# Kernel optimization log

Hardware: AMD Instinct MI355X
Metric: run time of the kernel (lower is better)

The kernel has to match this reference:

```python
import jax, jax.numpy as jnp
import numpy as np

N_NODES = 100000
N_EDGES = 200000
IN_FEATS = 1024
H_FEATS = 512
N_HEADS = 4
HEAD_DIM = H_FEATS // N_HEADS  # 128
N_CLASSES = 2983
BATCH = 1024


def setup_inputs() -> dict:
    key = jax.random.key(0)
    ks = jax.random.split(key, 24)
    x = jax.random.normal(ks[0], (N_NODES, IN_FEATS), jnp.float32)
    e1_src = jax.random.randint(ks[1], (N_EDGES,), 0, N_NODES)
    e1_dst = jax.random.randint(ks[2], (N_EDGES,), 0, N_NODES)
    e2_src = jax.random.randint(ks[3], (N_EDGES,), 0, N_NODES)
    e2_dst = jax.random.randint(ks[4], (N_EDGES,), 0, N_NODES)

    def lin_w(k, fin, fout):
        return jax.random.normal(k, (fin, fout), jnp.float32) * np.float32(1.0 / np.sqrt(fin))

    def att_w(k):
        return jax.random.normal(k, (N_HEADS, HEAD_DIM), jnp.float32) * np.float32(0.1)

    inp = dict(x=x, e1_src=e1_src, e1_dst=e1_dst, e2_src=e2_src, e2_dst=e2_dst,
               batch_size=BATCH)
    # layer 0 (in_feats -> h_feats), one GATConv per edge type
    inp["w0a"] = lin_w(ks[5], IN_FEATS, H_FEATS); inp["as0a"] = att_w(ks[6]); inp["ad0a"] = att_w(ks[7]); inp["b0a"] = jnp.zeros((H_FEATS,), jnp.float32)
    inp["w0b"] = lin_w(ks[8], IN_FEATS, H_FEATS); inp["as0b"] = att_w(ks[9]); inp["ad0b"] = att_w(ks[10]); inp["b0b"] = jnp.zeros((H_FEATS,), jnp.float32)
    # layer 1 (h_feats -> h_feats)
    inp["w1a"] = lin_w(ks[11], H_FEATS, H_FEATS); inp["as1a"] = att_w(ks[12]); inp["ad1a"] = att_w(ks[13]); inp["b1a"] = jnp.zeros((H_FEATS,), jnp.float32)
    inp["w1b"] = lin_w(ks[14], H_FEATS, H_FEATS); inp["as1b"] = att_w(ks[15]); inp["ad1b"] = att_w(ks[16]); inp["b1b"] = jnp.zeros((H_FEATS,), jnp.float32)
    # classification head
    inp["lin_w"] = lin_w(ks[17], H_FEATS, N_CLASSES)
    inp["lin_b"] = jnp.zeros((N_CLASSES,), jnp.float32)
    return inp


def gat_conv(x, src, dst, W, a_src, a_dst, b):
    """PyG GATConv (add_self_loops=False, concat=True, attn negative_slope=0.2)."""
    h = (x @ W).reshape(-1, N_HEADS, HEAD_DIM)          # [N, H, C]
    alpha_src = jnp.einsum('nhc,hc->nh', h, a_src)       # [N, H]
    alpha_dst = jnp.einsum('nhc,hc->nh', h, a_dst)       # [N, H]
    e = jax.nn.leaky_relu(alpha_src[src] + alpha_dst[dst], 0.2)   # [E, H]
    # segment softmax over incoming edges of each destination node
    m = jax.ops.segment_max(e, dst, num_segments=N_NODES)          # [N, H]
    ex = jnp.exp(e - m[dst])
    denom = jax.ops.segment_sum(ex, dst, num_segments=N_NODES)     # [N, H]
    alpha = ex / denom[dst]                                        # [E, H]
    msg = alpha[:, :, None] * h[src]                               # [E, H, C]
    out = jax.ops.segment_sum(msg, dst, num_segments=N_NODES)      # [N, H, C]
    return out.reshape(-1, N_HEADS * HEAD_DIM) + b


def reference(x, e1_src, e1_dst, e2_src, e2_dst, batch_size,
              w0a, as0a, ad0a, b0a, w0b, as0b, ad0b, b0b,
              w1a, as1a, ad1a, b1a, w1b, as1b, ad1b, b1b,
              lin_w, lin_b):
    # layer 0: HeteroConv sums per-edge-type GATConv outputs on 'paper'
    h1 = gat_conv(x, e1_src, e1_dst, w0a, as0a, ad0a, b0a) \
       + gat_conv(x, e2_src, e2_dst, w0b, as0b, ad0b, b0b)
    h1 = jax.nn.leaky_relu(h1, 0.01)   # F.leaky_relu default slope; dropout is identity in eval
    # layer 1
    h2 = gat_conv(h1, e1_src, e1_dst, w1a, as1a, ad1a, b1a) \
       + gat_conv(h1, e2_src, e2_dst, w1b, as1b, ad1b, b1b)
    # classification head on the seed nodes
    return h2[:batch_size] @ lin_w + lin_b
```

## Files before the change

### kernel.cpp

```cpp
#include <hip/hip_runtime.h>

#define N_NODES 100000
#define N_EDGES 200000
#define IN_FEATS 1024
#define H_FEATS 512
#define N_HEADS 4
#define HEAD_DIM 128
#define N_CLASSES 2983
#define BATCH 1024
#define NCHUNK2 782

typedef __attribute__((ext_vector_type(8))) short short8;
typedef __attribute__((ext_vector_type(4))) float floatx4;

typedef __attribute__((address_space(1))) void global_as_void;
typedef __attribute__((address_space(3))) void lds_as_void;

__device__ __forceinline__ float bf2f(unsigned short u) {
    union { unsigned int i; float f; } x; x.i = ((unsigned int)u) << 16; return x.f;
}
__device__ __forceinline__ unsigned short f2bf(float f) {
    union { float f; unsigned int i; } x; x.f = f;
    unsigned int r = x.i + 0x7FFFu + ((x.i >> 16) & 1u);
    return (unsigned short)(r >> 16);
}
__device__ __forceinline__ void load_lds16(const void* g, void* l) {
    __builtin_amdgcn_global_load_lds((const global_as_void*)g, (lds_as_void*)l, 16, 0, 0);
}

__global__ __launch_bounds__(256, 3)
void gemm_kernel(const void* __restrict__ Ain, int a_fp32, int a_dense,
                 const unsigned short* __restrict__ BT,
                 void* __restrict__ Cout, const float* __restrict__ bias,
                 const float* __restrict__ att_s, const float* __restrict__ att_d,
                 const float* __restrict__ att_s2, const float* __restrict__ att_d2,
                 float* __restrict__ asrc, float* __restrict__ adst,
                 const int* __restrict__ rowlist, const int* __restrict__ countp,
                 int M, int N, int n_tiles, int K, int out_bf16)
{
    __shared__ __attribute__((aligned(16))) unsigned short As[128 * 32];
    __shared__ __attribute__((aligned(16))) unsigned short Bs[128 * 32];
    __shared__ float attbuf[128][4];
    const int tid  = threadIdx.x;
    const int lane = tid & 63;
    const int wave = tid >> 6;
    const int bid = blockIdx.x;
    int mt, nt;
    if (n_tiles == 8) {
        mt = (bid & 7) + ((bid >> 6) << 3);
        nt = (bid >> 3) & 7;
    } else {
        mt = bid / n_tiles;
        nt = bid - mt * n_tiles;
    }
    const int m0 = mt * 128;
    const int n0 = nt * 128;
    int Mv = M;
    if (countp) Mv = countp[0];
    if (m0 >= Mv) return;
    const int wr = (wave >> 1) * 64;
    const int wc = (wave & 1) * 64;
    const int lm = lane & 15;
    const int quad = lane >> 4;

    auto arow = [&](int r) -> int {
        int gr = m0 + r; if (gr > Mv - 1) gr = Mv - 1;
        if (rowlist && !a_dense) gr = rowlist[gr];
        return gr;
    };

    const float* a_fp[2];
    const unsigned short* a_bf[2];
    char* a_lds[2];
    const unsigned short* b_bf[2];
    char* b_lds[2];
    if (a_fp32) {
        int row = tid >> 2, slot = tid & 3;
#pragma unroll
        for (int p = 0; p < 2; p++) {
            int r = p * 64 + row;
            a_fp[p] = (const float*)Ain + (size_t)arow(r) * K + (slot ^ ((r >> 1) & 3)) * 8;
        }
    } else {
#pragma unroll
        for (int i = 0; i < 2; i++) {
            int r = wave * 32 + i * 16 + (lane >> 2);
            a_bf[i] = (const unsigned short*)Ain + (size_t)arow(r) * K
                    + ((lane & 3) ^ ((r >> 1) & 3)) * 8;
            a_lds[i] = (char*)As + (size_t)(wave * 2 + i) * 1024;
        }
    }
#pragma unroll
    for (int i = 0; i < 2; i++) {
        int r = wave * 32 + i * 16 + (lane >> 2);
        int gn = n0 + r; if (gn > N - 1) gn = N - 1;
        b_bf[i] = BT + (size_t)gn * K + ((lane & 3) ^ ((r >> 1) & 3)) * 8;
        b_lds[i] = (char*)Bs + (size_t)(wave * 2 + i) * 1024;
    }

    floatx4 acc[4][4];
#pragma unroll
    for (int i = 0; i < 4; i++)
#pragma unroll
        for (int j = 0; j < 4; j++) acc[i][j] = (floatx4)0.0f;

    for (int k0 = 0; k0 < K; k0 += 32) {
        __syncthreads();
        if (a_fp32) {
            int row = tid >> 2, slot = tid & 3;
#pragma unroll
            for (int p = 0; p < 2; p++) {
                int r = p * 64 + row;
                floatx4 f0 = *(const floatx4*)(a_fp[p] + k0);
                floatx4 f1 = *(const floatx4*)(a_fp[p] + k0 + 4);
                short8 v;
                v[0] = (short)f2bf(f0[0]); v[1] = (short)f2bf(f0[1]);
                v[2] = (short)f2bf(f0[2]); v[3] = (short)f2bf(f0[3]);
                v[4] = (short)f2bf(f1[0]); v[5] = (short)f2bf(f1[1]);
                v[6] = (short)f2bf(f1[2]); v[7] = (short)f2bf(f1[3]);
                *(short8*)&As[r * 32 + slot * 8] = v;
            }
        } else {
#pragma unroll
            for (int i = 0; i < 2; i++)
                load_lds16(a_bf[i] + k0, a_lds[i]);
        }
#pragma unroll
        for (int i = 0; i < 2; i++)
            load_lds16(b_bf[i] + k0, b_lds[i]);
        __syncthreads();
        short8 af[4], bfr[4];
#pragma unroll
        for (int i = 0; i < 4; i++) {
            int ra = wr + i * 16 + lm;
            af[i] = *(const short8*)&As[ra * 32 + ((quad ^ ((ra >> 1) & 3)) << 3)];
            int rb = wc + i * 16 + lm;
            bfr[i] = *(const short8*)&Bs[rb * 32 + ((quad ^ ((rb >> 1) & 3)) << 3)];
        }
#pragma unroll
        for (int i = 0; i < 4; i++)
#pragma unroll
            for (int j = 0; j < 4; j++)
                acc[i][j] = __builtin_amdgcn_mfma_f32_16x16x32_bf16(af[i], bfr[j], acc[i][j], 0, 0, 0);
    }

    if (att_s) {
        const int h = nt;
        const float* wsp = (h < 4) ? att_s : att_s2;
        const float* wdp = (h < 4) ? att_d : att_d2;
        const int hh = h & 3;
        const int half2 = (wc >> 6) * 2;
#pragma unroll
        for (int i = 0; i < 4; i++) {
#pragma unroll
            for (int r = 0; r < 4; r++) {
                float ss = 0.f, sd = 0.f;
#pragma unroll
                for (int j = 0; j < 4; j++) {
                    int c = wc + j * 16 + lm;
                    ss += acc[i][j][r] * wsp[hh * HEAD_DIM + c];
                    sd += acc[i][j][r] * wdp[hh * HEAD_DIM + c];
                }
#pragma unroll
                for (int off = 1; off < 16; off <<= 1) {
                    ss += __shfl_xor(ss, off);
                    sd += __shfl_xor(sd, off);
                }
                if (lm == 0) {
                    int rl = wr + i * 16 + quad * 4 + r;
                    attbuf[rl][half2]     = ss;
                    attbuf[rl][half2 + 1] = sd;
                }
            }
        }
        __syncthreads();
        if (tid < 128) {
            int grl = m0 + tid;
            if (grl < Mv) {
                int gr = rowlist ? rowlist[grl] : grl;
                asrc[(size_t)gr * 8 + h] = attbuf[tid][0] + attbuf[tid][2];
                adst[(size_t)gr * 8 + h] = attbuf[tid][1] + attbuf[tid][3];
            }
        }
    }

#pragma unroll
    for (int i = 0; i < 4; i++) {
        int grb = wr + i * 16 + quad * 4;
#pragma unroll
        for (int j = 0; j < 4; j++) {
            int gc = n0 + wc + j * 16 + lm;
            if (gc < N) {
#pragma unroll
                for (int r = 0; r < 4; r++) {
                    int grl = m0 + grb + r;
                    if (grl < Mv) {
                        int gr = rowlist ? rowlist[grl] : grl;
                        float v = acc[i][j][r];
                        if (out_bf16) {
                            ((unsigned short*)Cout)[(size_t)gr * N + gc] = f2bf(v);
                        } else {
                            float b = bias ? bias[gc] : 0.0f;
                            ((float*)Cout)[(size_t)gr * N + gc] = v + b;
                        }
                    }
                }
            }
        }
    }
}

__global__ void prep1_kernel(const float* __restrict__ w0a, const float* __restrict__ w0b,
                             const float* __restrict__ w1a, const float* __restrict__ w1b,
                             const float* __restrict__ linw,
                             unsigned short* __restrict__ WT0, unsigned short* __restrict__ WT1,
                             unsigned short* __restrict__ WTl,
                             const int* __restrict__ e1s, const int* __restrict__ e1d,
                             const int* __restrict__ e2s, const int* __restrict__ e2d,
                             int* __restrict__ flag1, int* __restrict__ cnt2)
{
    const int gsz = gridDim.x * 256;
    const int gid = blockIdx.x * 256 + threadIdx.x;
    for (int i = gid; i < 1024 * 1024; i += gsz) {
        int n = i >> 10, k = i & 1023;
        const float* W = (n < 512) ? w0a : w0b;
        WT0[i] = f2bf(W[(size_t)k * 512 + (n & 511)]);
    }
    for (int i = gid; i < 1024 * 512; i += gsz) {
        int n = i >> 9, k = i & 511;
        const float* W = (n < 512) ? w1a : w1b;
        WT1[i] = f2bf(W[(size_t)k * 512 + (n & 511)]);
    }
    for (int i = gid; i < N_CLASSES * 512; i += gsz) {
        int n = i >> 9, k = i & 511;
        WTl[i] = f2bf(linw[(size_t)k * N_CLASSES + n]);
    }
    for (int e = gid; e < N_EDGES; e += gsz) {
        if (e < BATCH) flag1[e] = 1;
        int d1 = e1d[e], d2 = e2d[e];
        if (d1 < BATCH) flag1[e1s[e]] = 1;
        if (d2 < BATCH) flag1[e2s[e]] = 1;
        atomicAdd(&cnt2[d1], 1);
        atomicAdd(&cnt2[N_NODES + d2], 1);
    }
}

__global__ void mark0_kernel(const int* __restrict__ e1s, const int* __restrict__ e1d,
                             const int* __restrict__ e2s, const int* __restrict__ e2d,
                             const int* __restrict__ flag1, int* __restrict__ flag0,
                             int E, int Nn)
{
    int i = blockIdx.x * blockDim.x + threadIdx.x;
    if (i < E) {
        if (flag1[e1d[i]]) flag0[e1s[i]] = 1;
        if (flag1[e2d[i]]) flag0[e2s[i]] = 1;
    }
    if (i < Nn && flag1[i]) flag0[i] = 1;
}

__global__ void scanA_kernel(const int* __restrict__ flagbuf, const int* __restrict__ cnt2,
                             int* __restrict__ partialF, int* __restrict__ chunkF,
                             int* __restrict__ partialC, int* __restrict__ chunkC)
{
    __shared__ int sm[256];
    int b = blockIdx.x;
    const int* src; int* pdst; int* cdst; int cb;
    if (b < NCHUNK2) { src = flagbuf; pdst = partialF; cdst = chunkF; cb = b; }
    else             { src = cnt2;    pdst = partialC; cdst = chunkC; cb = b - NCHUNK2; }
    int t = threadIdx.x;
    int i = cb * 256 + t;
    int v = (i < 2 * N_NODES) ? src[i] : 0;
    sm[t] = v; __syncthreads();
    int val = v;
#pragma unroll
    for (int off = 1; off < 256; off <<= 1) {
        int u = (t >= off) ? sm[t - off] : 0;
        __syncthreads();
        val += u; sm[t] = val;
        __syncthreads();
    }
    if (i < 2 * N_NODES) pdst[i] = val - v;
    if (t == 255) cdst[cb] = val;
}

__global__ void scanB_kernel(int* __restrict__ chunkF, int* __restrict__ chunkC, int n)
{
    __shared__ int sm[1024];
    int t = threadIdx.x;
#pragma unroll
    for (int pass = 0; pass < 2; pass++) {
        int* c = pass ? chunkC : chunkF;
        int v = (t < n) ? c[t] : 0;
        sm[t] = v; __syncthreads();
        int val = v;
#pragma unroll
        for (int off = 1; off < 1024; off <<= 1) {
            int u = (t >= off) ? sm[t - off] : 0;
            __syncthreads();
            val += u; sm[t] = val;
            __syncthreads();
        }
        if (t < n) c[t] = val - v;
        __syncthreads();
    }
}

__global__ void finalize_kernel(const int* __restrict__ flagbuf,
                                const int* __restrict__ partialF, const int* __restrict__ chunkF,
                                const int* __restrict__ partialC, const int* __restrict__ chunkC,
                                int* __restrict__ list1, int* __restrict__ list0,
                                int* __restrict__ count1, int* __restrict__ count0,
                                int* __restrict__ rowptrc, int* __restrict__ cursor)
{
    int i = blockIdx.x * 256 + threadIdx.x;
    if (i >= 2 * N_NODES) return;
    int r = partialC[i] + chunkC[i >> 8];
    rowptrc[i] = r;
    cursor[i] = r;
    if (i == 0) rowptrc[2 * N_NODES] = 2 * N_EDGES;
    int total1 = partialF[N_NODES] + chunkF[N_NODES >> 8];
    int pos = partialF[i] + chunkF[i >> 8];
    int f = flagbuf[i];
    if (i < N_NODES) {
        if (f) list1[pos] = i;
        if (i == 0) count1[0] = total1;
    } else {
        if (f) list0[pos - total1] = i - N_NODES;
        if (i == 2 * N_NODES - 1) count0[0] = pos + f - total1;
    }
}

__global__ void fill_cvt_kernel(const int* __restrict__ e1s, const int* __restrict__ e1d,
                                const int* __restrict__ e2s, const int* __restrict__ e2d,
                                int* __restrict__ cursor, int* __restrict__ srcsc,
                                const float* __restrict__ X, const int* __restrict__ list0,
                                const int* __restrict__ count0, unsigned short* __restrict__ Y)
{
    const int gsz = gridDim.x * 256;
    const int gid = blockIdx.x * 256 + threadIdx.x;
    for (int e = gid; e < N_EDGES; e += gsz) {
        int p = atomicAdd(&cursor[e1d[e]], 1);
        srcsc[p] = e1s[e];
        int q = atomicAdd(&cursor[N_NODES + e2d[e]], 1);
        srcsc[q] = e2s[e];
    }
    int n0 = count0[0];
    int col = (threadIdx.x & 127) * 8;
    for (int i = blockIdx.x * 2 + (threadIdx.x >> 7); i < n0; i += gridDim.x * 2) {
        const floatx4* xp = (const floatx4*)(X + (size_t)list0[i] * IN_FEATS + col);
        floatx4 f0 = xp[0], f1 = xp[1];
        short8 v;
        v[0] = (short)f2bf(f0[0]); v[1] = (short)f2bf(f0[1]);
        v[2] = (short)f2bf(f0[2]); v[3] = (short)f2bf(f0[3]);
        v[4] = (short)f2bf(f1[0]); v[5] = (short)f2bf(f1[1]);
        v[6] = (short)f2bf(f1[2]); v[7] = (short)f2bf(f1[3]);
        *(short8*)(Y + (size_t)i * IN_FEATS + col) = v;
    }
}

__global__ void gather2_kernel(const int* __restrict__ rowptrc, const int* __restrict__ srcsc,
                               const float* __restrict__ asrc, const float* __restrict__ adst,
                               const unsigned short* __restrict__ H,
                               const float* __restrict__ b1, const float* __restrict__ b2,
                               const int* __restrict__ dlist, const int* __restrict__ dcountp,
                               unsigned short* __restrict__ Out, int ndst, int do_lrelu)
{
    int nd = dcountp ? dcountp[0] : ndst;
    int lane = threadIdx.x & 63;
    int head = lane >> 4;
    int col = lane * 8;
    for (int i = blockIdx.x * 4 + (threadIdx.x >> 6); i < nd; i += gridDim.x * 4) {
        int d = dlist ? dlist[i] : i;
        float r[8], acc[8];
        {
            int beg = rowptrc[d], end = rowptrc[d + 1];
            float ad = adst[(size_t)d * 8 + head];
            float den = 0.f;
#pragma unroll
            for (int k = 0; k < 8; k++) acc[k] = 0.f;
            for (int j = beg; j < end; j++) {
                int s = srcsc[j];
                float v = asrc[(size_t)s * 8 + head] + ad;
                v = v > 0.f ? v : 0.2f * v;
                float ex = expf(v);
                den += ex;
                short8 hv = *(const short8*)(H + (size_t)s * 1024 + col);
#pragma unroll
                for (int k = 0; k < 8; k++) acc[k] += ex * bf2f((unsigned short)hv[k]);
            }
            float inv = den > 0.f ? 1.f / den : 0.f;
#pragma unroll
            for (int k = 0; k < 8; k++) r[k] = acc[k] * inv;
        }
        {
            int beg = rowptrc[N_NODES + d], end = rowptrc[N_NODES + d + 1];
            float ad = adst[(size_t)d * 8 + 4 + head];
            float den = 0.f;
#pragma unroll
            for (int k = 0; k < 8; k++) acc[k] = 0.f;
            for (int j = beg; j < end; j++) {
                int s = srcsc[j];
                float v = asrc[(size_t)s * 8 + 4 + head] + ad;
                v = v > 0.f ? v : 0.2f * v;
                float ex = expf(v);
                den += ex;
                short8 hv = *(const short8*)(H + (size_t)s * 1024 + 512 + col);
#pragma unroll
                for (int k = 0; k < 8; k++) acc[k] += ex * bf2f((unsigned short)hv[k]);
            }
            float inv = den > 0.f ? 1.f / den : 0.f;
#pragma unroll
            for (int k = 0; k < 8; k++) r[k] += acc[k] * inv;
        }
        short8 o;
#pragma unroll
        for (int k = 0; k < 8; k++) {
            float f = r[k] + b1[col + k] + b2[col + k];
            if (do_lrelu) f = f > 0.f ? f : 0.01f * f;
            o[k] = (short)f2bf(f);
        }
        *(short8*)(Out + (size_t)i * 512 + col) = o;
    }
}

extern "C" void kernel_launch(void* const* d_in, const int* in_sizes, int n_in,
                              void* d_out, int out_size, void* d_ws, size_t ws_size,
                              hipStream_t stream)
{
    const float* x    = (const float*)d_in[0];
    const int* e1s    = (const int*)d_in[1];
    const int* e1d    = (const int*)d_in[2];
    const int* e2s    = (const int*)d_in[3];
    const int* e2d    = (const int*)d_in[4];
    const float* w0a  = (const float*)d_in[6];
    const float* as0a = (const float*)d_in[7];
    const float* ad0a = (const float*)d_in[8];
    const float* b0a  = (const float*)d_in[9];
    const float* w0b  = (const float*)d_in[10];
    const float* as0b = (const float*)d_in[11];
    const float* ad0b = (const float*)d_in[12];
    const float* b0b  = (const float*)d_in[13];
    const float* w1a  = (const float*)d_in[14];
    const float* as1a = (const float*)d_in[15];
    const float* ad1a = (const float*)d_in[16];
    const float* b1a  = (const float*)d_in[17];
    const float* w1b  = (const float*)d_in[18];
    const float* as1b = (const float*)d_in[19];
    const float* ad1b = (const float*)d_in[20];
    const float* b1b  = (const float*)d_in[21];
    const float* linw = (const float*)d_in[22];
    const float* linb = (const float*)d_in[23];
    float* out = (float*)d_out;
    (void)in_sizes; (void)n_in; (void)out_size;

    char* ws = (char*)d_ws;
    size_t off = 0;
    auto carve = [&](size_t bytes) -> void* {
        void* p = ws + off; off += (bytes + 255) & ~(size_t)255; return p;
    };
    unsigned short* WT0 = (unsigned short*)carve((size_t)2 * H_FEATS * IN_FEATS * 2);
    unsigned short* WT1 = (unsigned short*)carve((size_t)2 * H_FEATS * H_FEATS * 2);
    unsigned short* WTl = (unsigned short*)carve((size_t)N_CLASSES * H_FEATS * 2);
    unsigned short* Hbf = (unsigned short*)carve((size_t)N_NODES * 1024 * 2);
    unsigned short* H1c = (unsigned short*)carve((size_t)N_NODES * H_FEATS * 2);
    unsigned short* h2s = (unsigned short*)carve((size_t)BATCH * H_FEATS * 2);
    float* asrc = (float*)carve((size_t)N_NODES * 8 * 4);
    float* adst = (float*)carve((size_t)N_NODES * 8 * 4);
    int* cnt2    = (int*)carve((size_t)2 * N_NODES * 4);
    int* flagbuf = (int*)carve((size_t)2 * N_NODES * 4);
    int* rowptrc = (int*)carve((size_t)(2 * N_NODES + 1) * 4);
    int* srcsc   = (int*)carve((size_t)2 * N_EDGES * 4);
    int* partialF= (int*)carve((size_t)2 * N_NODES * 4);
    int* partialC= (int*)carve((size_t)2 * N_NODES * 4);
    int* chunkF  = (int*)carve((size_t)1024 * 4);
    int* chunkC  = (int*)carve((size_t)1024 * 4);
    int* list1   = (int*)carve((size_t)N_NODES * 4);
    int* list0   = (int*)carve((size_t)N_NODES * 4);
    int* count1  = (int*)carve(256);
    int* count0  = (int*)carve(256);
    unsigned short* xc = nullptr;
    {
        size_t need = (size_t)N_NODES * IN_FEATS * 2;
        if (off + need <= ws_size) xc = (unsigned short*)carve(need);
    }

    const int MT8 = (((N_NODES + 127) / 128) + 7) & ~7;
    const int EG = (N_EDGES + 255) / 256;

    hipMemsetAsync(cnt2, 0, (size_t)4 * N_NODES * 4, stream);
    prep1_kernel<<<2048, 256, 0, stream>>>(w0a, w0b, w1a, w1b, linw, WT0, WT1, WTl,
                                           e1s, e1d, e2s, e2d, flagbuf, cnt2);
    mark0_kernel<<<EG, 256, 0, stream>>>(e1s, e1d, e2s, e2d, flagbuf, flagbuf + N_NODES,
                                         N_EDGES, N_NODES);
    scanA_kernel<<<2 * NCHUNK2, 256, 0, stream>>>(flagbuf, cnt2, partialF, chunkF, partialC, chunkC);
    scanB_kernel<<<1, 1024, 0, stream>>>(chunkF, chunkC, NCHUNK2);
    finalize_kernel<<<NCHUNK2, 256, 0, stream>>>(flagbuf, partialF, chunkF, partialC, chunkC,
                                                 list1, list0, count1, count0, rowptrc, cnt2);
    fill_cvt_kernel<<<1024, 256, 0, stream>>>(e1s, e1d, e2s, e2d, cnt2, srcsc,
                                              x, list0, count0, xc ? xc : (unsigned short*)Hbf);

    if (xc) {
        gemm_kernel<<<MT8 * 8, 256, 0, stream>>>(xc, 0, 1, WT0, Hbf, nullptr,
                                                 as0a, ad0a, as0b, ad0b, asrc, adst,
                                                 list0, count0,
                                                 N_NODES, 1024, 8, IN_FEATS, 1);
    } else {
        gemm_kernel<<<MT8 * 8, 256, 0, stream>>>(x, 1, 0, WT0, Hbf, nullptr,
                                                 as0a, ad0a, as0b, ad0b, asrc, adst,
                                                 list0, count0,
                                                 N_NODES, 1024, 8, IN_FEATS, 1);
    }
    gather2_kernel<<<2048, 256, 0, stream>>>(rowptrc, srcsc, asrc, adst, Hbf, b0a, b0b,
                                             list1, count1, H1c, N_NODES, 1);
    gemm_kernel<<<MT8 * 8, 256, 0, stream>>>(H1c, 0, 1, WT1, Hbf, nullptr,
                                             as1a, ad1a, as1b, ad1b, asrc, adst,
                                             list1, count1,
                                             N_NODES, 1024, 8, H_FEATS, 1);
    gather2_kernel<<<256, 256, 0, stream>>>(rowptrc, srcsc, asrc, adst, Hbf, b1a, b1b,
                                            nullptr, nullptr, h2s, BATCH, 0);
    const int HN_T = (N_CLASSES + 127) / 128;
    gemm_kernel<<<(BATCH / 128) * HN_T, 256, 0, stream>>>(h2s, 0, 0, WTl, out, linb,
                                                          nullptr, nullptr, nullptr, nullptr,
                                                          nullptr, nullptr, nullptr, nullptr,
                                                          BATCH, N_CLASSES, HN_T, H_FEATS, 0);
}
```

Before: 749.0 us.

## Fuse preprocessing kernels into one cooperative kernel and double GEMM K-step

Six preprocessing launches plus a memset (weight transpose, flag marking, scans, CSR finalize, edge fill, x conversion) are merged into one cooperative kernel that separates phases with grid-wide syncs. This removes launch gaps and per-kernel tail effects. The GEMM main loop now loads two 32-wide K slices per iteration into doubled LDS buffers, halving the barrier count per tile. The trade-offs are more LDS per block, which may lower GEMM occupancy, and a 512-block cooperative grid that runs less parallel work in each phase than the old launches did.

```diff
diff --git a/kernel.cpp b/kernel.cpp
--- a/kernel.cpp
+++ b/kernel.cpp
@@ -1,4 +1,5 @@
 #include <hip/hip_runtime.h>
+#include <hip/hip_cooperative_groups.h>
 
 #define N_NODES 100000
 #define N_EDGES 200000
@@ -38,8 +39,8 @@
                  const int* __restrict__ rowlist, const int* __restrict__ countp,
                  int M, int N, int n_tiles, int K, int out_bf16)
 {
-    __shared__ __attribute__((aligned(16))) unsigned short As[128 * 32];
-    __shared__ __attribute__((aligned(16))) unsigned short Bs[128 * 32];
+    __shared__ __attribute__((aligned(16))) unsigned short As[2][128 * 32];
+    __shared__ __attribute__((aligned(16))) unsigned short Bs[2][128 * 32];
     __shared__ float attbuf[128][4];
     const int tid  = threadIdx.x;
     const int lane = tid & 63;
@@ -87,7 +88,7 @@
             int r = wave * 32 + i * 16 + (lane >> 2);
             a_bf[i] = (const unsigned short*)Ain + (size_t)arow(r) * K
                     + ((lane & 3) ^ ((r >> 1) & 3)) * 8;
-            a_lds[i] = (char*)As + (size_t)(wave * 2 + i) * 1024;
+            a_lds[i] = (char*)&As[0][0] + (size_t)(wave * 2 + i) * 1024;
         }
     }
 #pragma unroll
@@ -95,7 +96,7 @@
         int r = wave * 32 + i * 16 + (lane >> 2);
         int gn = n0 + r; if (gn > N - 1) gn = N - 1;
         b_bf[i] = BT + (size_t)gn * K + ((lane & 3) ^ ((r >> 1) & 3)) * 8;
-        b_lds[i] = (char*)Bs + (size_t)(wave * 2 + i) * 1024;
+        b_lds[i] = (char*)&Bs[0][0] + (size_t)(wave * 2 + i) * 1024;
     }
 
     floatx4 acc[4][4];
@@ -104,44 +105,54 @@
 #pragma unroll
         for (int j = 0; j < 4; j++) acc[i][j] = (floatx4)0.0f;
 
-    for (int k0 = 0; k0 < K; k0 += 32) {
+    for (int k0 = 0; k0 < K; k0 += 64) {
         __syncthreads();
         if (a_fp32) {
             int row = tid >> 2, slot = tid & 3;
 #pragma unroll
+            for (int pp = 0; pp < 2; pp++)
+#pragma unroll
             for (int p = 0; p < 2; p++) {
                 int r = p * 64 + row;
-                floatx4 f0 = *(const floatx4*)(a_fp[p] + k0);
-                floatx4 f1 = *(const floatx4*)(a_fp[p] + k0 + 4);
+                const float* ap = a_fp[p] + k0 + pp * 32;
+                floatx4 f0 = *(const floatx4*)ap;
+                floatx4 f1 = *(const floatx4*)(ap + 4);
                 short8 v;
                 v[0] = (short)f2bf(f0[0]); v[1] = (short)f2bf(f0[1]);
                 v[2] = (short)f2bf(f0[2]); v[3] = (short)f2bf(f0[3]);
                 v[4] = (short)f2bf(f1[0]); v[5] = (short)f2bf(f1[1]);
                 v[6] = (short)f2bf(f1[2]); v[7] = (short)f2bf(f1[3]);
-                *(short8*)&As[r * 32 + slot * 8] = v;
+                *(short8*)&As[pp][r * 32 + slot * 8] = v;
             }
         } else {
 #pragma unroll
+            for (int pp = 0; pp < 2; pp++)
+#pragma unroll
             for (int i = 0; i < 2; i++)
-                load_lds16(a_bf[i] + k0, a_lds[i]);
-        }
+                load_lds16(a_bf[i] + k0 + pp * 32, a_lds[i] + pp * 8192);
+        }
+#pragma unroll
+        for (int pp = 0; pp < 2; pp++)
 #pragma unroll
         for (int i = 0; i < 2; i++)
-            load_lds16(b_bf[i] + k0, b_lds[i]);
+            load_lds16(b_bf[i] + k0 + pp * 32, b_lds[i] + pp * 8192);
         __syncthreads();
-        short8 af[4], bfr[4];
-#pragma unroll
-        for (int i = 0; i < 4; i++) {
-            int ra = wr + i * 16 + lm;
-            af[i] = *(const short8*)&As[ra * 32 + ((quad ^ ((ra >> 1) & 3)) << 3)];
-            int rb = wc + i * 16 + lm;
-            bfr[i] = *(const short8*)&Bs[rb * 32 + ((quad ^ ((rb >> 1) & 3)) << 3)];
-        }
-#pragma unroll
-        for (int i = 0; i < 4; i++)
-#pragma unroll
-            for (int j = 0; j < 4; j++)
-                acc[i][j] = __builtin_amdgcn_mfma_f32_16x16x32_bf16(af[i], bfr[j], acc[i][j], 0, 0, 0);
+#pragma unroll
+        for (int pp = 0; pp < 2; pp++) {
+            short8 af[4], bfr[4];
+#pragma unroll
+            for (int i = 0; i < 4; i++) {
+                int ra = wr + i * 16 + lm;
+                af[i] = *(const short8*)&As[pp][ra * 32 + ((quad ^ ((ra >> 1) & 3)) << 3)];
+                int rb = wc + i * 16 + lm;
+                bfr[i] = *(const short8*)&Bs[pp][rb * 32 + ((quad ^ ((rb >> 1) & 3)) << 3)];
+            }
+#pragma unroll
+            for (int i = 0; i < 4; i++)
+#pragma unroll
+                for (int j = 0; j < 4; j++)
+                    acc[i][j] = __builtin_amdgcn_mfma_f32_16x16x32_bf16(af[i], bfr[j], acc[i][j], 0, 0, 0);
+        }
     }
 
     if (att_s) {
@@ -210,151 +221,145 @@
     }
 }
 
-__global__ void prep1_kernel(const float* __restrict__ w0a, const float* __restrict__ w0b,
-                             const float* __restrict__ w1a, const float* __restrict__ w1b,
-                             const float* __restrict__ linw,
-                             unsigned short* __restrict__ WT0, unsigned short* __restrict__ WT1,
-                             unsigned short* __restrict__ WTl,
-                             const int* __restrict__ e1s, const int* __restrict__ e1d,
-                             const int* __restrict__ e2s, const int* __restrict__ e2d,
-                             int* __restrict__ flag1, int* __restrict__ cnt2)
+struct PrepArgs {
+    const float *w0a, *w0b, *w1a, *w1b, *linw;
+    unsigned short *WT0, *WT1, *WTl;
+    const int *e1s, *e1d, *e2s, *e2d;
+    int *flagbuf, *cnt2;
+    int *partialF, *chunkF, *partialC, *chunkC;
+    int *list1, *list0, *count1, *count0;
+    int *rowptrc, *srcsc;
+    const float* x;
+    unsigned short* xc;
+};
+
+__global__ __launch_bounds__(256, 2)
+void prep_all_kernel(PrepArgs a)
 {
+    cooperative_groups::grid_group g = cooperative_groups::this_grid();
     const int gsz = gridDim.x * 256;
     const int gid = blockIdx.x * 256 + threadIdx.x;
+    const int t = threadIdx.x;
+    __shared__ int sm[1024];
+    __shared__ int ts[256];
+
+    for (int i = gid; i < 4 * N_NODES; i += gsz) a.cnt2[i] = 0;
+    g.sync();
+
     for (int i = gid; i < 1024 * 1024; i += gsz) {
         int n = i >> 10, k = i & 1023;
-        const float* W = (n < 512) ? w0a : w0b;
-        WT0[i] = f2bf(W[(size_t)k * 512 + (n & 511)]);
+        const float* W = (n < 512) ? a.w0a : a.w0b;
+        a.WT0[i] = f2bf(W[(size_t)k * 512 + (n & 511)]);
     }
     for (int i = gid; i < 1024 * 512; i += gsz) {
         int n = i >> 9, k = i & 511;
-        const float* W = (n < 512) ? w1a : w1b;
-        WT1[i] = f2bf(W[(size_t)k * 512 + (n & 511)]);
+        const float* W = (n < 512) ? a.w1a : a.w1b;
+        a.WT1[i] = f2bf(W[(size_t)k * 512 + (n & 511)]);
     }
     for (int i = gid; i < N_CLASSES * 512; i += gsz) {
         int n = i >> 9, k = i & 511;
-        WTl[i] = f2bf(linw[(size_t)k * N_CLASSES + n]);
+        a.WTl[i] = f2bf(a.linw[(size_t)k * N_CLASSES + n]);
     }
     for (int e = gid; e < N_EDGES; e += gsz) {
-        if (e < BATCH) flag1[e] = 1;
-        int d1 = e1d[e], d2 = e2d[e];
-        if (d1 < BATCH) flag1[e1s[e]] = 1;
-        if (d2 < BATCH) flag1[e2s[e]] = 1;
-        atomicAdd(&cnt2[d1], 1);
-        atomicAdd(&cnt2[N_NODES + d2], 1);
-    }
-}
-
-__global__ void mark0_kernel(const int* __restrict__ e1s, const int* __restrict__ e1d,
-                             const int* __restrict__ e2s, const int* __restrict__ e2d,
-                             const int* __restrict__ flag1, int* __restrict__ flag0,
-                             int E, int Nn)
-{
-    int i = blockIdx.x * blockDim.x + threadIdx.x;
-    if (i < E) {
-        if (flag1[e1d[i]]) flag0[e1s[i]] = 1;
-        if (flag1[e2d[i]]) flag0[e2s[i]] = 1;
-    }
-    if (i < Nn && flag1[i]) flag0[i] = 1;
-}
-
-__global__ void scanA_kernel(const int* __restrict__ flagbuf, const int* __restrict__ cnt2,
-                             int* __restrict__ partialF, int* __restrict__ chunkF,
-                             int* __restrict__ partialC, int* __restrict__ chunkC)
-{
-    __shared__ int sm[256];
-    int b = blockIdx.x;
-    const int* src; int* pdst; int* cdst; int cb;
-    if (b < NCHUNK2) { src = flagbuf; pdst = partialF; cdst = chunkF; cb = b; }
-    else             { src = cnt2;    pdst = partialC; cdst = chunkC; cb = b - NCHUNK2; }
-    int t = threadIdx.x;
-    int i = cb * 256 + t;
-    int v = (i < 2 * N_NODES) ? src[i] : 0;
-    sm[t] = v; __syncthreads();
-    int val = v;
-#pragma unroll
-    for (int off = 1; off < 256; off <<= 1) {
-        int u = (t >= off) ? sm[t - off] : 0;
-        __syncthreads();
-        val += u; sm[t] = val;
-        __syncthreads();
-    }
-    if (i < 2 * N_NODES) pdst[i] = val - v;
-    if (t == 255) cdst[cb] = val;
-}
-
-__global__ void scanB_kernel(int* __restrict__ chunkF, int* __restrict__ chunkC, int n)
-{
-    __shared__ int sm[1024];
-    int t = threadIdx.x;
-#pragma unroll
-    for (int pass = 0; pass < 2; pass++) {
-        int* c = pass ? chunkC : chunkF;
-        int v = (t < n) ? c[t] : 0;
+        if (e < BATCH) a.flagbuf[e] = 1;
+        int d1 = a.e1d[e], d2 = a.e2d[e];
+        if (d1 < BATCH) a.flagbuf[a.e1s[e]] = 1;
+        if (d2 < BATCH) a.flagbuf[a.e2s[e]] = 1;
+        atomicAdd(&a.cnt2[d1], 1);
+        atomicAdd(&a.cnt2[N_NODES + d2], 1);
+    }
+    g.sync();
+
+    for (int e = gid; e < N_EDGES; e += gsz) {
+        if (a.flagbuf[a.e1d[e]]) a.flagbuf[N_NODES + a.e1s[e]] = 1;
+        if (a.flagbuf[a.e2d[e]]) a.flagbuf[N_NODES + a.e2s[e]] = 1;
+    }
+    for (int i = gid; i < N_NODES; i += gsz)
+        if (a.flagbuf[i]) a.flagbuf[N_NODES + i] = 1;
+    g.sync();
+
+    for (int c = blockIdx.x; c < 2 * NCHUNK2; c += gridDim.x) {
+        const int* src; int* pdst; int* cdst; int cb;
+        if (c < NCHUNK2) { src = a.flagbuf; pdst = a.partialF; cdst = a.chunkF; cb = c; }
+        else             { src = a.cnt2;    pdst = a.partialC; cdst = a.chunkC; cb = c - NCHUNK2; }
+        int i = cb * 256 + t;
+        int v = (i < 2 * N_NODES) ? src[i] : 0;
         sm[t] = v; __syncthreads();
         int val = v;
 #pragma unroll
-        for (int off = 1; off < 1024; off <<= 1) {
+        for (int off = 1; off < 256; off <<= 1) {
             int u = (t >= off) ? sm[t - off] : 0;
             __syncthreads();
             val += u; sm[t] = val;
             __syncthreads();
         }
-        if (t < n) c[t] = val - v;
+        if (i < 2 * N_NODES) pdst[i] = val - v;
+        if (t == 255) cdst[cb] = val;
         __syncthreads();
     }
-}
-
-__global__ void finalize_kernel(const int* __restrict__ flagbuf,
-                                const int* __restrict__ partialF, const int* __restrict__ chunkF,
-                                const int* __restrict__ partialC, const int* __restrict__ chunkC,
-                                int* __restrict__ list1, int* __restrict__ list0,
-                                int* __restrict__ count1, int* __restrict__ count0,
-                                int* __restrict__ rowptrc, int* __restrict__ cursor)
-{
-    int i = blockIdx.x * 256 + threadIdx.x;
-    if (i >= 2 * N_NODES) return;
-    int r = partialC[i] + chunkC[i >> 8];
-    rowptrc[i] = r;
-    cursor[i] = r;
-    if (i == 0) rowptrc[2 * N_NODES] = 2 * N_EDGES;
-    int total1 = partialF[N_NODES] + chunkF[N_NODES >> 8];
-    int pos = partialF[i] + chunkF[i >> 8];
-    int f = flagbuf[i];
-    if (i < N_NODES) {
-        if (f) list1[pos] = i;
-        if (i == 0) count1[0] = total1;
-    } else {
-        if (f) list0[pos - total1] = i - N_NODES;
-        if (i == 2 * N_NODES - 1) count0[0] = pos + f - total1;
-    }
-}
-
-__global__ void fill_cvt_kernel(const int* __restrict__ e1s, const int* __restrict__ e1d,
-                                const int* __restrict__ e2s, const int* __restrict__ e2d,
-                                int* __restrict__ cursor, int* __restrict__ srcsc,
-                                const float* __restrict__ X, const int* __restrict__ list0,
-                                const int* __restrict__ count0, unsigned short* __restrict__ Y)
-{
-    const int gsz = gridDim.x * 256;
-    const int gid = blockIdx.x * 256 + threadIdx.x;
+    g.sync();
+
+    if (blockIdx.x == 0) {
+        for (int pass = 0; pass < 2; pass++) {
+            int* c = pass ? a.chunkC : a.chunkF;
+            for (int i = t; i < 1024; i += 256) sm[i] = (i < NCHUNK2) ? c[i] : 0;
+            __syncthreads();
+            int b4 = t * 4;
+            int a0 = sm[b4], a1 = sm[b4 + 1], a2 = sm[b4 + 2], a3 = sm[b4 + 3];
+            int s1 = a0, s2 = s1 + a1, s3 = s2 + a2, tot = s3 + a3;
+            ts[t] = tot; __syncthreads();
+            int val = tot;
+#pragma unroll
+            for (int off = 1; off < 256; off <<= 1) {
+                int u = (t >= off) ? ts[t - off] : 0;
+                __syncthreads();
+                val += u; ts[t] = val;
+                __syncthreads();
+            }
+            int exc = val - tot;
+            sm[b4] = exc; sm[b4 + 1] = exc + s1; sm[b4 + 2] = exc + s2; sm[b4 + 3] = exc + s3;
+            __syncthreads();
+            for (int i = t; i < NCHUNK2; i += 256) c[i] = sm[i];
+            __syncthreads();
+        }
+    }
+    g.sync();
+
+    for (int i = gid; i < 2 * N_NODES; i += gsz) {
+        int r = a.partialC[i] + a.chunkC[i >> 8];
+        a.rowptrc[i] = r;
+        a.cnt2[i] = r;
+        if (i == 0) a.rowptrc[2 * N_NODES] = 2 * N_EDGES;
+        int total1 = a.partialF[N_NODES] + a.chunkF[N_NODES >> 8];
+        int pos = a.partialF[i] + a.chunkF[i >> 8];
+        int f = a.flagbuf[i];
+        if (i < N_NODES) {
+            if (f) a.list1[pos] = i;
+            if (i == 0) a.count1[0] = total1;
+        } else {
+            if (f) a.list0[pos - total1] = i - N_NODES;
+            if (i == 2 * N_NODES - 1) a.count0[0] = pos + f - total1;
+        }
+    }
+    g.sync();
+
     for (int e = gid; e < N_EDGES; e += gsz) {
-        int p = atomicAdd(&cursor[e1d[e]], 1);
-        srcsc[p] = e1s[e];
-        int q = atomicAdd(&cursor[N_NODES + e2d[e]], 1);
-        srcsc[q] = e2s[e];
-    }
-    int n0 = count0[0];
-    int col = (threadIdx.x & 127) * 8;
-    for (int i = blockIdx.x * 2 + (threadIdx.x >> 7); i < n0; i += gridDim.x * 2) {
-        const floatx4* xp = (const floatx4*)(X + (size_t)list0[i] * IN_FEATS + col);
+        int p = atomicAdd(&a.cnt2[a.e1d[e]], 1);
+        a.srcsc[p] = a.e1s[e];
+        int q = atomicAdd(&a.cnt2[N_NODES + a.e2d[e]], 1);
+        a.srcsc[q] = a.e2s[e];
+    }
+    int n0 = a.count0[0];
+    int col = (t & 127) * 8;
+    for (int i = blockIdx.x * 2 + (t >> 7); i < n0; i += gridDim.x * 2) {
+        const floatx4* xp = (const floatx4*)(a.x + (size_t)a.list0[i] * IN_FEATS + col);
         floatx4 f0 = xp[0], f1 = xp[1];
         short8 v;
         v[0] = (short)f2bf(f0[0]); v[1] = (short)f2bf(f0[1]);
         v[2] = (short)f2bf(f0[2]); v[3] = (short)f2bf(f0[3]);
         v[4] = (short)f2bf(f1[0]); v[5] = (short)f2bf(f1[1]);
         v[6] = (short)f2bf(f1[2]); v[7] = (short)f2bf(f1[3]);
-        *(short8*)(Y + (size_t)i * IN_FEATS + col) = v;
+        *(short8*)(a.xc + (size_t)i * IN_FEATS + col) = v;
     }
 }
 
@@ -485,19 +490,21 @@
     }
 
     const int MT8 = (((N_NODES + 127) / 128) + 7) & ~7;
-    const int EG = (N_EDGES + 255) / 256;
-
-    hipMemsetAsync(cnt2, 0, (size_t)4 * N_NODES * 4, stream);
-    prep1_kernel<<<2048, 256, 0, stream>>>(w0a, w0b, w1a, w1b, linw, WT0, WT1, WTl,
-                                           e1s, e1d, e2s, e2d, flagbuf, cnt2);
-    mark0_kernel<<<EG, 256, 0, stream>>>(e1s, e1d, e2s, e2d, flagbuf, flagbuf + N_NODES,
-                                         N_EDGES, N_NODES);
-    scanA_kernel<<<2 * NCHUNK2, 256, 0, stream>>>(flagbuf, cnt2, partialF, chunkF, partialC, chunkC);
-    scanB_kernel<<<1, 1024, 0, stream>>>(chunkF, chunkC, NCHUNK2);
-    finalize_kernel<<<NCHUNK2, 256, 0, stream>>>(flagbuf, partialF, chunkF, partialC, chunkC,
-                                                 list1, list0, count1, count0, rowptrc, cnt2);
-    fill_cvt_kernel<<<1024, 256, 0, stream>>>(e1s, e1d, e2s, e2d, cnt2, srcsc,
-                                              x, list0, count0, xc ? xc : (unsigned short*)Hbf);
+
+    {
+        PrepArgs pa;
+        pa.w0a = w0a; pa.w0b = w0b; pa.w1a = w1a; pa.w1b = w1b; pa.linw = linw;
+        pa.WT0 = WT0; pa.WT1 = WT1; pa.WTl = WTl;
+        pa.e1s = e1s; pa.e1d = e1d; pa.e2s = e2s; pa.e2d = e2d;
+        pa.flagbuf = flagbuf; pa.cnt2 = cnt2;
+        pa.partialF = partialF; pa.chunkF = chunkF; pa.partialC = partialC; pa.chunkC = chunkC;
+        pa.list1 = list1; pa.list0 = list0; pa.count1 = count1; pa.count0 = count0;
+        pa.rowptrc = rowptrc; pa.srcsc = srcsc;
+        pa.x = x; pa.xc = xc ? xc : (unsigned short*)Hbf;
+        void* params[] = { &pa };
+        hipLaunchCooperativeKernel((void*)prep_all_kernel, dim3(512), dim3(256),
+                                   params, 0, stream);
+    }
 
     if (xc) {
         gemm_kernel<<<MT8 * 8, 256, 0, stream>>>(xc, 0, 1, WT0, Hbf, nullptr,
```

After: 1.100 ms. 1.47x slower.
